# Optimization experiments

Hardware: AMD Instinct MI355X
Metric: run time of the kernel (lower is better)

Reference implementation:

```python
import jax, jax.numpy as jnp
import numpy as np

D = 1152      # hidden_size
H = 16        # num_heads
K = D // H    # head_dim = 72
L = 2         # depth
I = 4304      # intermediate_size
M = 2         # spatial_merge_size
NPOS = 2304   # num_position_embeddings (48x48)
OUT = 2048    # out_hidden_size
CIN = 3 * 2 * 16 * 16  # C*tp*p*p = 1536
GRID = np.array([[1, 48, 48], [1, 32, 64], [2, 24, 40]], dtype=np.int32)


def _ln(x, s, b, eps=1e-6):
    mu = jnp.mean(x, -1, keepdims=True)
    var = jnp.mean((x - mu) ** 2, -1, keepdims=True)
    return (x - mu) * jax.lax.rsqrt(var + eps) * s + b


def _rot_half(x):
    h = x.shape[-1] // 2
    return jnp.concatenate([-x[..., h:], x[..., :h]], -1)


def _seg_bounds(g):
    b = [0]
    for t, h, w in g:
        for _ in range(int(t)):
            b.append(b[-1] + int(h) * int(w))
    return list(zip(b[:-1], b[1:]))


def _rope_cos_sin(g):
    half = K // 2  # rotary_half_dim
    max_hw = int(g[:, 1:].max())
    inv = 1.0 / (10000.0 ** (np.arange(0, half, 2, dtype=np.float64) / half))
    table = np.arange(max_hw)[:, None] * inv[None, :]  # (max_hw, half//2)
    pos = []
    for t, h, w in g:
        t, h, w = int(t), int(h), int(w)
        mh, mw = h // M, w // M
        row = np.broadcast_to(np.arange(mh)[:, None, None, None] * M + np.arange(M)[None, None, :, None], (mh, mw, M, M)).reshape(-1)
        col = np.broadcast_to(np.arange(mw)[None, :, None, None] * M + np.arange(M)[None, None, None, :], (mh, mw, M, M)).reshape(-1)
        c = np.stack([row, col], -1)
        if t > 1:
            c = np.tile(c, (t, 1))
        pos.append(c)
    pos = np.concatenate(pos, 0)
    emb = table[pos].reshape(pos.shape[0], -1)     # (N, half)
    emb = np.concatenate([emb, emb], -1)           # (N, head_dim)
    return jnp.asarray(np.cos(emb), jnp.float32), jnp.asarray(np.sin(emb), jnp.float32)


def _pos_embeds(pos_table, g):
    n = int(NPOS ** 0.5)
    outs = []
    for t, h, w in g:
        t, h, w = int(t), int(h), int(w)
        hi = np.linspace(0, n - 1, h); wi = np.linspace(0, n - 1, w)
        hf = np.floor(hi).astype(np.int32); wf = np.floor(wi).astype(np.int32)
        hc = np.clip(hf + 1, 0, n - 1); wc = np.clip(wf + 1, 0, n - 1)
        dh = (hi - hf).astype(np.float32); dw = (wi - wf).astype(np.float32)
        i00 = (hf[:, None] * n + wf[None, :]).reshape(-1)
        i01 = (hf[:, None] * n + wc[None, :]).reshape(-1)
        i10 = (hc[:, None] * n + wf[None, :]).reshape(-1)
        i11 = (hc[:, None] * n + wc[None, :]).reshape(-1)
        w00 = ((1 - dh)[:, None] * (1 - dw)[None, :]).reshape(-1, 1)
        w01 = ((1 - dh)[:, None] * dw[None, :]).reshape(-1, 1)
        w10 = (dh[:, None] * (1 - dw)[None, :]).reshape(-1, 1)
        w11 = (dh[:, None] * dw[None, :]).reshape(-1, 1)
        e = pos_table[i00] * w00 + pos_table[i01] * w01 + pos_table[i10] * w10 + pos_table[i11] * w11
        # spatial-merge reorder
        e = jnp.tile(e, (t, 1)).reshape(t, h // M, M, w // M, M, -1).transpose(0, 1, 3, 2, 4, 5).reshape(-1, D)
        outs.append(e)
    return jnp.concatenate(outs, 0)


def _forward(pixel_values, grid, patch_w, patch_b, pos_table, ln1_s, ln1_b, qkv_w, qkv_b,
             proj_w, proj_b, ln2_s, ln2_b, fc1_w, fc1_b, fc2_w, fc2_b,
             m_ln_s, m_ln_b, m_fc1_w, m_fc1_b, m_fc2_w, m_fc2_b):
    g = np.asarray(grid)
    # patch embed: conv with kernel==stride over whole patch == matmul on flattened patch
    x = pixel_values @ patch_w + patch_b               # (N, D)
    x = x + _pos_embeds(pos_table, g)
    cos, sin = _rope_cos_sin(g)                        # (N, K) each
    bounds = _seg_bounds(g)
    scale = K ** -0.5
    for l in range(L):
        h = _ln(x, ln1_s[l], ln1_b[l])
        N = h.shape[0]
        qkv = (h @ qkv_w[l] + qkv_b[l]).reshape(N, 3, H, K)
        q, k, v = qkv[:, 0], qkv[:, 1], qkv[:, 2]
        q = q * cos[:, None, :] + _rot_half(q) * sin[:, None, :]
        k = k * cos[:, None, :] + _rot_half(k) * sin[:, None, :]
        outs = []
        for s, e in bounds:  # static ragged segments (cu_seqlens)
            logits = jnp.einsum('lhk,mhk->hlm', q[s:e], k[s:e]) * scale
            wts = jax.nn.softmax(logits.astype(jnp.float32), -1).astype(logits.dtype)
            outs.append(jnp.einsum('hlm,mhk->lhk', wts, v[s:e]).reshape(e - s, H * K))
        attn = jnp.concatenate(outs, 0) @ proj_w[l] + proj_b[l]
        x = x + attn
        h2 = _ln(x, ln2_s[l], ln2_b[l])
        x = x + jax.nn.gelu(h2 @ fc1_w[l] + fc1_b[l], approximate=True) @ fc2_w[l] + fc2_b[l]
    normed = _ln(x, m_ln_s, m_ln_b).reshape(-1, D * M * M)
    return jax.nn.gelu(normed @ m_fc1_w + m_fc1_b, approximate=True) @ m_fc2_w + m_fc2_b


def setup_inputs() -> dict:
    key = jax.random.key(0)
    ks = jax.random.split(key, 16)
    def nrm(k, shp, s=0.02):
        return jax.random.normal(k, shp, jnp.float32) * s
    Ntok = int(sum(int(t) * int(h) * int(w) for t, h, w in GRID))  # 6272
    return {
        'pixel_values': nrm(ks[0], (Ntok, CIN), 1.0),
        'grid_thw': jnp.asarray(GRID),
        'patch_w': nrm(ks[1], (CIN, D)), 'patch_b': nrm(ks[2], (D,), 0.01),
        'pos_table': nrm(ks[3], (NPOS, D)),
        'ln1_s': jnp.ones((L, D)), 'ln1_b': jnp.zeros((L, D)),
        'qkv_w': nrm(ks[4], (L, D, 3 * D)), 'qkv_b': nrm(ks[5], (L, 3 * D), 0.01),
        'proj_w': nrm(ks[6], (L, D, D)), 'proj_b': nrm(ks[7], (L, D), 0.01),
        'ln2_s': jnp.ones((L, D)), 'ln2_b': jnp.zeros((L, D)),
        'fc1_w': nrm(ks[8], (L, D, I)), 'fc1_b': nrm(ks[9], (L, I), 0.01),
        'fc2_w': nrm(ks[10], (L, I, D)), 'fc2_b': nrm(ks[11], (L, D), 0.01),
        'm_ln_s': jnp.ones((D,)), 'm_ln_b': jnp.zeros((D,)),
        'm_fc1_w': nrm(ks[12], (D * M * M, D * M * M)), 'm_fc1_b': nrm(ks[13], (D * M * M,), 0.01),
        'm_fc2_w': nrm(ks[14], (D * M * M, OUT)), 'm_fc2_b': nrm(ks[15], (OUT,), 0.01),
    }


def reference(pixel_values, grid_thw, patch_w, patch_b, pos_table, ln1_s, ln1_b, qkv_w, qkv_b,
              proj_w, proj_b, ln2_s, ln2_b, fc1_w, fc1_b, fc2_w, fc2_b,
              m_ln_s, m_ln_b, m_fc1_w, m_fc1_b, m_fc2_w, m_fc2_b):
    return _forward(pixel_values, grid_thw, patch_w, patch_b, pos_table, ln1_s, ln1_b, qkv_w, qkv_b,
                    proj_w, proj_b, ln2_s, ln2_b, fc1_w, fc1_b, fc2_w, fc2_b,
                    m_ln_s, m_ln_b, m_fc1_w, m_fc1_b, m_fc2_w, m_fc2_b)
```

## Files before the change

kernel.cpp:

```cpp
#include <hip/hip_runtime.h>

typedef __bf16 bf16;
typedef float f32x4 __attribute__((ext_vector_type(4)));
typedef bf16 bf16x8 __attribute__((ext_vector_type(8)));

#define NTOK 6272
#define DMODEL 1152

__device__ __forceinline__ void tok_geo(int t, int& row, int& col, int& gh, int& gw) {
    int local;
    if (t < 2304)      { local = t;        gh = 48; gw = 48; }
    else if (t < 4352) { local = t - 2304; gh = 32; gw = 64; }
    else if (t < 5312) { local = t - 4352; gh = 24; gw = 40; }
    else               { local = t - 5312; gh = 24; gw = 40; }
    int mc = local & 1;
    int mr = (local >> 1) & 1;
    int rest = local >> 2;
    int mwc = gw >> 1;
    int mw = rest % mwc;
    int mh = rest / mwc;
    row = mh * 2 + mr;
    col = mw * 2 + mc;
}

__device__ __forceinline__ float gelu_tanh(float v) {
    float c = v + 0.044715f * v * v * v;
    return 0.5f * v * (1.0f + tanhf(0.7978845608028654f * c));
}

__global__ void detect_kernel(const unsigned short* __restrict__ px, int* __restrict__ flag) {
    int tid = threadIdx.x;
    int cnt = 0;
    for (int i = tid * 8; i < tid * 8 + 8; i++) {
        unsigned e = (px[i] >> 7) & 0xFF;
        if (e < 100u || e > 140u) cnt++;
    }
#pragma unroll
    for (int off = 32; off > 0; off >>= 1) cnt += __shfl_down(cnt, off);
    if (tid == 0) *flag = (cnt > 64) ? 1 : 0;
}

template <typename T>
__device__ __forceinline__ void load8(const T* src, bf16* dst, bool pred) {
    if (!pred) {
        uint4 z = {0, 0, 0, 0};
        *(uint4*)dst = z;
        return;
    }
    if constexpr (sizeof(T) == 2) {
        *(uint4*)dst = *(const uint4*)src;
    } else {
        float4 a = *(const float4*)src;
        float4 b = *(const float4*)(src + 4);
        dst[0] = (bf16)a.x; dst[1] = (bf16)a.y; dst[2] = (bf16)a.z; dst[3] = (bf16)a.w;
        dst[4] = (bf16)b.x; dst[5] = (bf16)b.y; dst[6] = (bf16)b.z; dst[7] = (bf16)b.w;
    }
}

template <typename TI>
__global__ __launch_bounds__(256) void pos_embed_kernel(const int* __restrict__ flag,
                                                        const TI* __restrict__ tab,
                                                        bf16* __restrict__ x) {
    if (*flag != (sizeof(TI) == 4 ? 1 : 0)) return;
    int t = blockIdx.x;
    int row, col, gh, gw;
    tok_geo(t, row, col, gh, gw);
    float hi = row * 47.0f / (gh - 1);
    float wi = col * 47.0f / (gw - 1);
    int hf = (int)hi, wf = (int)wi;
    int hc = min(hf + 1, 47), wc = min(wf + 1, 47);
    float dh = hi - hf, dw = wi - wf;
    float w00 = (1.f - dh) * (1.f - dw);
    float w01 = (1.f - dh) * dw;
    float w10 = dh * (1.f - dw);
    float w11 = dh * dw;
    const TI* p00 = tab + (size_t)(hf * 48 + wf) * DMODEL;
    const TI* p01 = tab + (size_t)(hf * 48 + wc) * DMODEL;
    const TI* p10 = tab + (size_t)(hc * 48 + wf) * DMODEL;
    const TI* p11 = tab + (size_t)(hc * 48 + wc) * DMODEL;
    bf16* xr = x + (size_t)t * DMODEL;
    for (int d = threadIdx.x; d < DMODEL; d += 256)
        xr[d] = (bf16)(w00 * (float)p00[d] + w01 * (float)p01[d] +
                       w10 * (float)p10[d] + w11 * (float)p11[d]);
}

template <typename TI>
__global__ __launch_bounds__(256) void ln_kernel(const int* __restrict__ flag,
                                                 const bf16* __restrict__ x,
                                                 const TI* __restrict__ s,
                                                 const TI* __restrict__ b,
                                                 bf16* __restrict__ out) {
    if (*flag != (sizeof(TI) == 4 ? 1 : 0)) return;
    const int row = blockIdx.x;
    const int tid = threadIdx.x;
    __shared__ float red[4];
    const bf16* xr = x + (size_t)row * DMODEL;
    float vals[5];
    int cnt = 0;
    float sum = 0.f;
    for (int i = tid; i < DMODEL; i += 256) { vals[cnt] = (float)xr[i]; sum += vals[cnt]; cnt++; }
#pragma unroll
    for (int off = 32; off > 0; off >>= 1) sum += __shfl_down(sum, off);
    if ((tid & 63) == 0) red[tid >> 6] = sum;
    __syncthreads();
    float mean = (red[0] + red[1] + red[2] + red[3]) * (1.0f / DMODEL);
    float vs = 0.f;
    for (int i = 0; i < cnt; i++) { float d = vals[i] - mean; vs += d * d; }
#pragma unroll
    for (int off = 32; off > 0; off >>= 1) vs += __shfl_down(vs, off);
    __syncthreads();
    if ((tid & 63) == 0) red[tid >> 6] = vs;
    __syncthreads();
    float var = (red[0] + red[1] + red[2] + red[3]) * (1.0f / DMODEL);
    float inv = rsqrtf(var + 1e-6f);
    int idx = 0;
    for (int i = tid; i < DMODEL; i += 256)
        out[(size_t)row * DMODEL + i] = (bf16)((vals[idx++] - mean) * inv * (float)s[i] + (float)b[i]);
}

__global__ __launch_bounds__(256) void rope_inplace_kernel(bf16* __restrict__ qkv) {
    int idx = blockIdx.x * 256 + threadIdx.x;
    const int total = NTOK * 16 * 36;
    if (idx >= total) return;
    int j = idx % 36;
    int rest = idx / 36;
    int h = rest & 15;
    int t = rest >> 4;
    bf16* base = qkv + (size_t)t * 3456 + h * 72;
    int row, col, gh, gw;
    tok_geo(t, row, col, gh, gw);
    float pos = (float)((j < 18) ? row : col);
    int fi = (j < 18) ? j : j - 18;
    float ang = pos * powf(10000.0f, -(float)fi / 18.0f);
    float cv = cosf(ang), sv = sinf(ang);
    float q0v = (float)base[j],        q1v = (float)base[j + 36];
    float k0v = (float)base[1152 + j], k1v = (float)base[1152 + j + 36];
    base[j]          = (bf16)(q0v * cv - q1v * sv);
    base[j + 36]     = (bf16)(q1v * cv + q0v * sv);
    base[1152 + j]      = (bf16)(k0v * cv - k1v * sv);
    base[1152 + j + 36] = (bf16)(k1v * cv + k0v * sv);
}

__global__ __launch_bounds__(256) void attn_kernel(const bf16* __restrict__ qkv,
                                                   bf16* __restrict__ outp) {
    const int bx = blockIdx.x;
    const int head = bx & 15;
    const int qt = bx >> 4;
    int sbase, slen, qtb;
    if (qt < 36)      { sbase = 0;    slen = 2304; qtb = 0;  }
    else if (qt < 68) { sbase = 2304; slen = 2048; qtb = 36; }
    else if (qt < 83) { sbase = 4352; slen = 960;  qtb = 68; }
    else              { sbase = 5312; slen = 960;  qtb = 83; }
    const int q0 = sbase + (qt - qtb) * 64;

    __shared__ bf16 Ks[64][104];
    __shared__ bf16 Vs[80][72];
    __shared__ bf16 Ps[64][72];

    const int tid = threadIdx.x;
    const int wv = tid >> 6;
    const int lane = tid & 63;
    const int quad = lane >> 4;
    const int l15 = lane & 15;

    const size_t hoff = (size_t)head * 72;

    for (int c = tid; c < 64; c += 256) {
        int r = 72 + (c >> 3), cc = (c & 7) * 8;
        uint4 z = {0, 0, 0, 0};
        *(uint4*)&Vs[r][cc] = z;
    }

    for (int c = tid; c < 768; c += 256) {
        int r = c / 12, cc = (c % 12) * 8;
        uint4 v = {0, 0, 0, 0};
        if (cc < 72) v = *(const uint4*)(qkv + (size_t)(q0 + r) * 3456 + hoff + cc);
        *(uint4*)&Ks[r][cc] = v;
    }
    __syncthreads();
    bf16x8 aq[3];
#pragma unroll
    for (int i = 0; i < 3; i++) aq[i] = *(const bf16x8*)&Ks[wv * 16 + l15][i * 32 + quad * 8];

    const int cc0 = wv * 8;
    const bool w0 = tid < 64;
    const bf16* kp = qkv + (size_t)(sbase + lane) * 3456 + 1152 + hoff + cc0;
    const int stepE = 64 * 3456;

    uint4 kr0, kr1, kr2, vr0, vr1, vr2;
    kr0 = *(const uint4*)kp;
    kr1 = *(const uint4*)(kp + 32);
    vr0 = *(const uint4*)(kp + 1152);
    vr1 = *(const uint4*)(kp + 1184);
    if (w0) {
        kr2 = *(const uint4*)(kp + 64);
        vr2 = *(const uint4*)(kp + 1216);
    }
    kp += stepE;

    f32x4 o[5] = {};
    float m_i[4], l_i[4];
#pragma unroll
    for (int r = 0; r < 4; r++) { m_i[r] = -1e30f; l_i[r] = 0.f; }

    const float C1 = 0.17002234f;
    const int nkv = slen >> 6;
    for (int kt = 0; kt < nkv; kt++) {
        __syncthreads();
        *(uint4*)&Ks[lane][cc0] = kr0;
        *(uint4*)&Ks[lane][cc0 + 32] = kr1;
        if (w0) *(uint4*)&Ks[lane][64] = kr2;
        {
            const bf16* e = (const bf16*)&vr0;
#pragma unroll
            for (int i = 0; i < 8; i++) Vs[cc0 + i][lane] = e[i];
        }
        {
            const bf16* e = (const bf16*)&vr1;
#pragma unroll
            for (int i = 0; i < 8; i++) Vs[cc0 + 32 + i][lane] = e[i];
        }
        if (w0) {
            const bf16* e = (const bf16*)&vr2;
#pragma unroll
            for (int i = 0; i < 8; i++) Vs[64 + i][lane] = e[i];
        }
        __syncthreads();

        if (kt + 1 < nkv) {
            kr0 = *(const uint4*)kp;
            kr1 = *(const uint4*)(kp + 32);
            vr0 = *(const uint4*)(kp + 1152);
            vr1 = *(const uint4*)(kp + 1184);
            if (w0) {
                kr2 = *(const uint4*)(kp + 64);
                vr2 = *(const uint4*)(kp + 1216);
            }
            kp += stepE;
        }

        f32x4 sfr[4] = {};
#pragma unroll
        for (int kc = 0; kc < 3; kc++)
#pragma unroll
            for (int nt = 0; nt < 4; nt++) {
                bf16x8 bk = *(const bf16x8*)&Ks[nt * 16 + l15][kc * 32 + quad * 8];
                sfr[nt] = __builtin_amdgcn_mfma_f32_16x16x32_bf16(aq[kc], bk, sfr[nt], 0, 0, 0);
            }

        float mx[4];
#pragma unroll
        for (int reg = 0; reg < 4; reg++) {
            float m = fmaxf(fmaxf(sfr[0][reg], sfr[1][reg]), fmaxf(sfr[2][reg], sfr[3][reg]));
            m = fmaxf(m, __shfl_xor(m, 1));
            m = fmaxf(m, __shfl_xor(m, 2));
            m = fmaxf(m, __shfl_xor(m, 4));
            m = fmaxf(m, __shfl_xor(m, 8));
            mx[reg] = m;
        }
        bool grow = (mx[0] > m_i[0]) || (mx[1] > m_i[1]) || (mx[2] > m_i[2]) || (mx[3] > m_i[3]);
        if (__any(grow)) {
#pragma unroll
            for (int reg = 0; reg < 4; reg++) {
                float mn = fmaxf(m_i[reg], mx[reg]);
                float a = __builtin_amdgcn_exp2f((m_i[reg] - mn) * C1);
                m_i[reg] = mn;
                l_i[reg] *= a;
#pragma unroll
                for (int nt = 0; nt < 5; nt++) o[nt][reg] *= a;
            }
        }
        float mc[4];
#pragma unroll
        for (int reg = 0; reg < 4; reg++) mc[reg] = m_i[reg] * C1;
        float rs[4] = {0.f, 0.f, 0.f, 0.f};
#pragma unroll
        for (int nt = 0; nt < 4; nt++)
#pragma unroll
            for (int reg = 0; reg < 4; reg++) {
                float p = __builtin_amdgcn_exp2f(fmaf(sfr[nt][reg], C1, -mc[reg]));
                sfr[nt][reg] = p;
                rs[reg] += p;
            }
#pragma unroll
        for (int reg = 0; reg < 4; reg++) {
            float r = rs[reg];
            r += __shfl_xor(r, 1);
            r += __shfl_xor(r, 2);
            r += __shfl_xor(r, 4);
            r += __shfl_xor(r, 8);
            l_i[reg] += r;
        }

#pragma unroll
        for (int nt = 0; nt < 4; nt++)
#pragma unroll
            for (int reg = 0; reg < 4; reg++)
                Ps[wv * 16 + quad * 4 + reg][nt * 16 + l15] = (bf16)sfr[nt][reg];

#pragma unroll
        for (int kc = 0; kc < 2; kc++) {
            bf16x8 ap = *(const bf16x8*)&Ps[wv * 16 + l15][kc * 32 + quad * 8];
#pragma unroll
            for (int nt = 0; nt < 5; nt++) {
                bf16x8 bv = *(const bf16x8*)&Vs[nt * 16 + l15][kc * 32 + quad * 8];
                o[nt] = __builtin_amdgcn_mfma_f32_16x16x32_bf16(ap, bv, o[nt], 0, 0, 0);
            }
        }
    }

#pragma unroll
    for (int nt = 0; nt < 5; nt++)
#pragma unroll
        for (int reg = 0; reg < 4; reg++) {
            int c = nt * 16 + l15;
            if (c < 72) {
                int tok = q0 + wv * 16 + quad * 4 + reg;
                outp[(size_t)tok * DMODEL + head * 72 + c] = (bf16)(o[nt][reg] / l_i[reg]);
            }
        }
}

template <int MODE, typename TA, typename TB>
__global__ __launch_bounds__(256) void gemm_kernel(const int* __restrict__ flag,
                                                   const TA* __restrict__ A,
                                                   const TB* __restrict__ B,
                                                   const TB* __restrict__ bias,
                                                   void* __restrict__ outp,
                                                   int M, int N, int K) {
    if (*flag != (sizeof(TB) == 4 ? 1 : 0)) return;
    __shared__ bf16 As[128][40];
    __shared__ bf16 Bs[128][40];
    const int tid = threadIdx.x;
    const int m0 = blockIdx.y * 128;
    const int n0 = blockIdx.x * 128;
    const int wv = tid >> 6;
    const int lane = tid & 63;
    const int quad = lane >> 4;
    const int l15 = lane & 15;
    const int wr = (wv >> 1) * 64;
    const int wc = (wv & 1) * 64;

    const int a_row = tid >> 1;
    const int a_col = (tid & 1) * 16;
    const int b_k = tid & 31;
    const int b_n = (tid >> 5) * 16;

    f32x4 acc[4][4] = {};

    for (int k0 = 0; k0 < K; k0 += 32) {
        __syncthreads();
        {
            bf16 ea[16];
            int gr = m0 + a_row;
            const TA* ap = A + (size_t)gr * K + k0 + a_col;
            load8(ap, ea, gr < M && (k0 + a_col) < K);
            load8(ap + 8, ea + 8, gr < M && (k0 + a_col + 8) < K);
            *(uint4*)&As[a_row][a_col] = *(uint4*)ea;
            *(uint4*)&As[a_row][a_col + 8] = *(uint4*)(ea + 8);
        }
        {
            bf16 eb[16];
            int gk = k0 + b_k;
            const TB* bp = B + (size_t)gk * N + n0 + b_n;
            load8(bp, eb, gk < K && (n0 + b_n) < N);
            load8(bp + 8, eb + 8, gk < K && (n0 + b_n + 8) < N);
#pragma unroll
            for (int i = 0; i < 16; i++) Bs[b_n + i][b_k] = eb[i];
        }
        __syncthreads();

        bf16x8 af[4], bfv[4];
#pragma unroll
        for (int mi = 0; mi < 4; mi++) af[mi] = *(const bf16x8*)&As[wr + mi * 16 + l15][quad * 8];
#pragma unroll
        for (int ni = 0; ni < 4; ni++) bfv[ni] = *(const bf16x8*)&Bs[wc + ni * 16 + l15][quad * 8];
#pragma unroll
        for (int mi = 0; mi < 4; mi++)
#pragma unroll
            for (int ni = 0; ni < 4; ni++)
                acc[mi][ni] = __builtin_amdgcn_mfma_f32_16x16x32_bf16(af[mi], bfv[ni], acc[mi][ni], 0, 0, 0);
    }

#pragma unroll
    for (int mi = 0; mi < 4; mi++) {
#pragma unroll
        for (int ni = 0; ni < 4; ni++) {
#pragma unroll
            for (int reg = 0; reg < 4; reg++) {
                int r = m0 + wr + mi * 16 + quad * 4 + reg;
                int c = n0 + wc + ni * 16 + l15;
                if (r < M && c < N) {
                    float v = acc[mi][ni][reg] + (float)bias[c];
                    if (MODE == 1) v = gelu_tanh(v);
                    if (MODE == 2) {
                        bf16* o = (bf16*)outp;
                        size_t idx = (size_t)r * N + c;
                        o[idx] = (bf16)((float)o[idx] + v);
                    } else if (MODE == 3) {
                        TB* o = (TB*)outp;
                        o[(size_t)r * N + c] = (TB)v;
                    } else {
                        bf16* o = (bf16*)outp;
                        o[(size_t)r * N + c] = (bf16)v;
                    }
                }
            }
        }
    }
}


template <typename TI>
__global__ __launch_bounds__(256) void cvt_kernel(const int* __restrict__ flag,
                                                  const TI* __restrict__ in,
                                                  bf16* __restrict__ out, int n8) {
    if (*flag != (sizeof(TI) == 4 ? 1 : 0)) return;
    for (int i = blockIdx.x * 256 + threadIdx.x; i < n8; i += gridDim.x * 256) {
        bf16 e[8];
        load8(in + (size_t)i * 8, e, true);
        *(uint4*)(out + (size_t)i * 8) = *(uint4*)e;
    }
}

template <typename TI>
__global__ __launch_bounds__(256) void transpose_w_kernel(const int* __restrict__ flag,
                                                          const TI* __restrict__ B,
                                                          bf16* __restrict__ T,
                                                          int K, int N, int Kpad) {
    if (*flag != (sizeof(TI) == 4 ? 1 : 0)) return;
    __shared__ bf16 t[64][72];
    const int k0 = blockIdx.y * 64, n0 = blockIdx.x * 64;
    const int tid = threadIdx.x;
    const int kk = tid >> 2;
    const int nn0 = (tid & 3) * 16;
    bf16 e[16];
    bool ok = (k0 + kk < K) && (n0 + nn0 < N);
    const TI* src = B + (size_t)(k0 + kk) * N + n0 + nn0;
    load8(src, e, ok);
    load8(src + 8, e + 8, ok);
#pragma unroll
    for (int i = 0; i < 16; i++) t[nn0 + i][kk] = e[i];
    __syncthreads();
    const int nn = tid >> 2;
    const int j16 = (tid & 3) * 16;
    if (n0 + nn < N && k0 + j16 < Kpad) {
        bf16* dst = T + (size_t)(n0 + nn) * Kpad + k0 + j16;
        *(uint4*)dst = *(uint4*)&t[nn][j16];
        *(uint4*)(dst + 8) = *(uint4*)&t[nn][j16 + 8];
    }
}

template <typename TI>
__global__ __launch_bounds__(256) void cvt_bias_kernel(const int* __restrict__ flag,
        const TI* p0, const TI* p1, const TI* p2, const TI* p3, const TI* p4,
        const TI* p5, const TI* p6, const TI* p7, const TI* p8, const TI* p9,
        const TI* p10, bf16* __restrict__ out) {
    if (*flag != (sizeof(TI) == 4 ? 1 : 0)) return;
    const int lens[11] = {1152, 3456, 3456, 1152, 1152, 4304, 4304, 1152, 1152, 4608, 2048};
    const int offs[11] = {0, 1152, 4608, 8064, 9216, 10368, 14672, 18976, 20128, 21280, 25888};
    int b = blockIdx.x;
    const TI* src = (b == 0) ? p0 : (b == 1) ? p1 : (b == 2) ? p2 : (b == 3) ? p3
                  : (b == 4) ? p4 : (b == 5) ? p5 : (b == 6) ? p6 : (b == 7) ? p7
                  : (b == 8) ? p8 : (b == 9) ? p9 : p10;
    for (int i = threadIdx.x; i < lens[b]; i += 256) out[offs[b] + i] = (bf16)(float)src[i];
}

typedef const __attribute__((address_space(1))) void* gas_ptr;
typedef __attribute__((address_space(3))) void* las_ptr;
__device__ __forceinline__ void gload16(const bf16* g, bf16* l) {
    __builtin_amdgcn_global_load_lds((gas_ptr)g, (las_ptr)l, 16, 0, 0);
}

template <int MODE>
__global__ __launch_bounds__(256) void gemm_lds_kernel(const int* __restrict__ flag,
        const bf16* __restrict__ A, const bf16* __restrict__ BT,
        const bf16* __restrict__ bias, void* __restrict__ outp,
        int M, int N, int K, int ldc) {
    __shared__ bf16 As[128][32];
    __shared__ bf16 Bs[128][32];
    const int tid = threadIdx.x;
    const int m0 = blockIdx.y * 128;
    const int n0 = blockIdx.x * 128;
    const int wv = tid >> 6;
    const int lane = tid & 63;
    const int quad = lane >> 4;
    const int l15 = lane & 15;
    const int wr = (wv >> 1) * 64;
    const int wc = (wv & 1) * 64;

    const int sr = wv * 32 + (lane >> 2);
    const int sc = (lane & 3) * 8;
    const bf16* aP0 = A + (size_t)min(m0 + sr, M - 1) * K + sc;
    const bf16* aP1 = A + (size_t)min(m0 + sr + 16, M - 1) * K + sc;
    const bf16* bP0 = BT + (size_t)min(n0 + sr, N - 1) * K + sc;
    const bf16* bP1 = BT + (size_t)min(n0 + sr + 16, N - 1) * K + sc;
    bf16* lA0 = &As[wv * 32][0];
    bf16* lA1 = &As[wv * 32 + 16][0];
    bf16* lB0 = &Bs[wv * 32][0];
    bf16* lB1 = &Bs[wv * 32 + 16][0];

    f32x4 acc[4][4] = {};
    for (int k0 = 0; k0 < K; k0 += 32) {
        __syncthreads();
        gload16(aP0 + k0, lA0);
        gload16(aP1 + k0, lA1);
        gload16(bP0 + k0, lB0);
        gload16(bP1 + k0, lB1);
        __syncthreads();
        bf16x8 af[4], bfv[4];
#pragma unroll
        for (int mi = 0; mi < 4; mi++) af[mi] = *(const bf16x8*)&As[wr + mi * 16 + l15][quad * 8];
#pragma unroll
        for (int ni = 0; ni < 4; ni++) bfv[ni] = *(const bf16x8*)&Bs[wc + ni * 16 + l15][quad * 8];
#pragma unroll
        for (int mi = 0; mi < 4; mi++)
#pragma unroll
            for (int ni = 0; ni < 4; ni++)
                acc[mi][ni] = __builtin_amdgcn_mfma_f32_16x16x32_bf16(af[mi], bfv[ni], acc[mi][ni], 0, 0, 0);
    }

    const int isf32 = (MODE == 3) ? *flag : 0;
#pragma unroll
    for (int mi = 0; mi < 4; mi++) {
#pragma unroll
        for (int ni = 0; ni < 4; ni++) {
#pragma unroll
            for (int reg = 0; reg < 4; reg++) {
                int r = m0 + wr + mi * 16 + quad * 4 + reg;
                int c = n0 + wc + ni * 16 + l15;
                if (r < M && c < ldc) {
                    float v = 0.f;
                    if (c < N) {
                        v = acc[mi][ni][reg] + (float)bias[c];
                        if (MODE == 1) v = gelu_tanh(v);
                    }
                    if (MODE == 2) {
                        bf16* o = (bf16*)outp;
                        size_t idx = (size_t)r * ldc + c;
                        o[idx] = (bf16)((float)o[idx] + v);
                    } else if (MODE == 3) {
                        if (isf32) ((float*)outp)[(size_t)r * ldc + c] = v;
                        else       ((bf16*)outp)[(size_t)r * ldc + c] = (bf16)v;
                    } else {
                        ((bf16*)outp)[(size_t)r * ldc + c] = (bf16)v;
                    }
                }
            }
        }
    }
}

#define OFF_PATCH  0ULL
#define OFF_QKV    1769472ULL
#define QKV_SZ     3981312ULL
#define OFF_PROJ   9732096ULL
#define PROJ_SZ    1327104ULL
#define OFF_FC1    12386304ULL
#define FC1_SZ     4958208ULL
#define OFF_FC2    22302720ULL
#define FC2_SZ     4976640ULL
#define OFF_MFC1   32256000ULL
#define OFF_MFC2   53489664ULL
#define OFF_BIAS   62926848ULL
#define WS_NEEDED  209001280ULL

extern "C" void kernel_launch(void* const* d_in, const int* in_sizes, int n_in,
                              void* d_out, int out_size, void* d_ws, size_t ws_size,
                              hipStream_t stream) {
    char* ws = (char*)d_ws;
    int* flag  = (int*)ws;
    bf16* x    = (bf16*)(ws + 256);
    bf16* h    = (bf16*)(ws + 256 + 14450688);
    bf16* bufA = (bf16*)(ws + 256 + 28901376);

    detect_kernel<<<1, 64, 0, stream>>>((const unsigned short*)d_in[0], flag);

    if (ws_size >= WS_NEEDED) {
        bf16* wT = (bf16*)(ws + 256 + 28901376 + 54190080);
        bf16* bias = wT + OFF_BIAS;
        bf16* px = bufA;

        cvt_kernel<bf16><<<1024, 256, 0, stream>>>(flag, (const bf16*)d_in[0], px, 1204224);
        cvt_kernel<float><<<1024, 256, 0, stream>>>(flag, (const float*)d_in[0], px, 1204224);

        auto T2 = [&](const void* srcBase, size_t eoff, bf16* dst, int K, int N, int Kpad) {
            dim3 g((N + 63) / 64, (Kpad + 63) / 64);
            transpose_w_kernel<bf16><<<g, 256, 0, stream>>>(flag, (const bf16*)srcBase + eoff, dst, K, N, Kpad);
            transpose_w_kernel<float><<<g, 256, 0, stream>>>(flag, (const float*)srcBase + eoff, dst, K, N, Kpad);
        };
        T2(d_in[2], 0, wT + OFF_PATCH, 1536, 1152, 1536);
        for (int l = 0; l < 2; l++) {
            T2(d_in[7],  (size_t)l * 1152 * 3456, wT + OFF_QKV + l * QKV_SZ, 1152, 3456, 1152);
            T2(d_in[9],  (size_t)l * 1152 * 1152, wT + OFF_PROJ + l * PROJ_SZ, 1152, 1152, 1152);
            T2(d_in[13], (size_t)l * 1152 * 4304, wT + OFF_FC1 + l * FC1_SZ, 1152, 4304, 1152);
            T2(d_in[15], (size_t)l * 4304 * 1152, wT + OFF_FC2 + l * FC2_SZ, 4304, 1152, 4320);
        }
        T2(d_in[19], 0, wT + OFF_MFC1, 4608, 4608, 4608);
        T2(d_in[21], 0, wT + OFF_MFC2, 4608, 2048, 4608);

        cvt_bias_kernel<bf16><<<11, 256, 0, stream>>>(flag,
            (const bf16*)d_in[3],
            (const bf16*)d_in[8], (const bf16*)d_in[8] + 3456,
            (const bf16*)d_in[10], (const bf16*)d_in[10] + 1152,
            (const bf16*)d_in[14], (const bf16*)d_in[14] + 4304,
            (const bf16*)d_in[16], (const bf16*)d_in[16] + 1152,
            (const bf16*)d_in[20], (const bf16*)d_in[22], bias);
        cvt_bias_kernel<float><<<11, 256, 0, stream>>>(flag,
            (const float*)d_in[3],
            (const float*)d_in[8], (const float*)d_in[8] + 3456,
            (const float*)d_in[10], (const float*)d_in[10] + 1152,
            (const float*)d_in[14], (const float*)d_in[14] + 4304,
            (const float*)d_in[16], (const float*)d_in[16] + 1152,
            (const float*)d_in[20], (const float*)d_in[22], bias);

        pos_embed_kernel<bf16><<<NTOK, 256, 0, stream>>>(flag, (const bf16*)d_in[4], x);
        pos_embed_kernel<float><<<NTOK, 256, 0, stream>>>(flag, (const float*)d_in[4], x);

        gemm_lds_kernel<2><<<dim3(9, 49), 256, 0, stream>>>(flag, px, wT + OFF_PATCH,
                                                            bias + 0, x, NTOK, 1152, 1536, 1152);

        for (int l = 0; l < 2; l++) {
            ln_kernel<bf16><<<NTOK, 256, 0, stream>>>(flag, x, (const bf16*)d_in[5] + l * 1152,
                                                      (const bf16*)d_in[6] + l * 1152, h);
            ln_kernel<float><<<NTOK, 256, 0, stream>>>(flag, x, (const float*)d_in[5] + l * 1152,
                                                       (const float*)d_in[6] + l * 1152, h);
            gemm_lds_kernel<0><<<dim3(27, 49), 256, 0, stream>>>(flag, h, wT + OFF_QKV + l * QKV_SZ,
                                                                 bias + 1152 + l * 3456, bufA,
                                                                 NTOK, 3456, 1152, 3456);
            rope_inplace_kernel<<<(NTOK * 16 * 36 + 255) / 256, 256, 0, stream>>>(bufA);
            attn_kernel<<<98 * 16, 256, 0, stream>>>(bufA, h);
            gemm_lds_kernel<2><<<dim3(9, 49), 256, 0, stream>>>(flag, h, wT + OFF_PROJ + l * PROJ_SZ,
                                                                bias + 8064 + l * 1152, x,
                                                                NTOK, 1152, 1152, 1152);
            ln_kernel<bf16><<<NTOK, 256, 0, stream>>>(flag, x, (const bf16*)d_in[11] + l * 1152,
                                                      (const bf16*)d_in[12] + l * 1152, h);
            ln_kernel<float><<<NTOK, 256, 0, stream>>>(flag, x, (const float*)d_in[11] + l * 1152,
                                                       (const float*)d_in[12] + l * 1152, h);
            gemm_lds_kernel<1><<<dim3(34, 49), 256, 0, stream>>>(flag, h, wT + OFF_FC1 + l * FC1_SZ,
                                                                 bias + 10368 + l * 4304, bufA,
                                                                 NTOK, 4304, 1152, 4320);
            gemm_lds_kernel<2><<<dim3(9, 49), 256, 0, stream>>>(flag, bufA, wT + OFF_FC2 + l * FC2_SZ,
                                                                bias + 18976 + l * 1152, x,
                                                                NTOK, 1152, 4320, 1152);
        }
        ln_kernel<bf16><<<NTOK, 256, 0, stream>>>(flag, x, (const bf16*)d_in[17], (const bf16*)d_in[18], h);
        ln_kernel<float><<<NTOK, 256, 0, stream>>>(flag, x, (const float*)d_in[17], (const float*)d_in[18], h);
        gemm_lds_kernel<1><<<dim3(36, 13), 256, 0, stream>>>(flag, h, wT + OFF_MFC1,
                                                             bias + 21280, bufA, 1568, 4608, 4608, 4608);
        gemm_lds_kernel<3><<<dim3(16, 13), 256, 0, stream>>>(flag, bufA, wT + OFF_MFC2,
                                                             bias + 25888, d_out, 1568, 2048, 4608, 2048);
        return;
    }

    {
        pos_embed_kernel<bf16><<<NTOK, 256, 0, stream>>>(flag, (const bf16*)d_in[4], x);
        pos_embed_kernel<float><<<NTOK, 256, 0, stream>>>(flag, (const float*)d_in[4], x);
        gemm_kernel<2, bf16, bf16><<<dim3(9, 49), 256, 0, stream>>>(
            flag, (const bf16*)d_in[0], (const bf16*)d_in[2], (const bf16*)d_in[3], x, NTOK, 1152, 1536);
        gemm_kernel<2, float, float><<<dim3(9, 49), 256, 0, stream>>>(
            flag, (const float*)d_in[0], (const float*)d_in[2], (const float*)d_in[3], x, NTOK, 1152, 1536);
    }
    for (int l = 0; l < 2; l++) {
        ln_kernel<bf16><<<NTOK, 256, 0, stream>>>(flag, x, (const bf16*)d_in[5] + l * 1152,
                                                  (const bf16*)d_in[6] + l * 1152, h);
        ln_kernel<float><<<NTOK, 256, 0, stream>>>(flag, x, (const float*)d_in[5] + l * 1152,
                                                   (const float*)d_in[6] + l * 1152, h);
        gemm_kernel<0, bf16, bf16><<<dim3(27, 49), 256, 0, stream>>>(
            flag, h, (const bf16*)d_in[7] + (size_t)l * 1152 * 3456,
            (const bf16*)d_in[8] + l * 3456, bufA, NTOK, 3456, 1152);
        gemm_kernel<0, bf16, float><<<dim3(27, 49), 256, 0, stream>>>(
            flag, h, (const float*)d_in[7] + (size_t)l * 1152 * 3456,
            (const float*)d_in[8] + l * 3456, bufA, NTOK, 3456, 1152);
        rope_inplace_kernel<<<(NTOK * 16 * 36 + 255) / 256, 256, 0, stream>>>(bufA);
        attn_kernel<<<98 * 16, 256, 0, stream>>>(bufA, h);
        gemm_kernel<2, bf16, bf16><<<dim3(9, 49), 256, 0, stream>>>(
            flag, h, (const bf16*)d_in[9] + (size_t)l * 1152 * 1152,
            (const bf16*)d_in[10] + l * 1152, x, NTOK, 1152, 1152);
        gemm_kernel<2, bf16, float><<<dim3(9, 49), 256, 0, stream>>>(
            flag, h, (const float*)d_in[9] + (size_t)l * 1152 * 1152,
            (const float*)d_in[10] + l * 1152, x, NTOK, 1152, 1152);
        ln_kernel<bf16><<<NTOK, 256, 0, stream>>>(flag, x, (const bf16*)d_in[11] + l * 1152,
                                                  (const bf16*)d_in[12] + l * 1152, h);
        ln_kernel<float><<<NTOK, 256, 0, stream>>>(flag, x, (const float*)d_in[11] + l * 1152,
                                                   (const float*)d_in[12] + l * 1152, h);
        gemm_kernel<1, bf16, bf16><<<dim3(34, 49), 256, 0, stream>>>(
            flag, h, (const bf16*)d_in[13] + (size_t)l * 1152 * 4304,
            (const bf16*)d_in[14] + l * 4304, bufA, NTOK, 4304, 1152);
        gemm_kernel<1, bf16, float><<<dim3(34, 49), 256, 0, stream>>>(
            flag, h, (const float*)d_in[13] + (size_t)l * 1152 * 4304,
            (const float*)d_in[14] + l * 4304, bufA, NTOK, 4304, 1152);
        gemm_kernel<2, bf16, bf16><<<dim3(9, 49), 256, 0, stream>>>(
            flag, bufA, (const bf16*)d_in[15] + (size_t)l * 4304 * 1152,
            (const bf16*)d_in[16] + l * 1152, x, NTOK, 1152, 4304);
        gemm_kernel<2, bf16, float><<<dim3(9, 49), 256, 0, stream>>>(
            flag, bufA, (const float*)d_in[15] + (size_t)l * 4304 * 1152,
            (const float*)d_in[16] + l * 1152, x, NTOK, 1152, 4304);
    }
    ln_kernel<bf16><<<NTOK, 256, 0, stream>>>(flag, x, (const bf16*)d_in[17], (const bf16*)d_in[18], h);
    ln_kernel<float><<<NTOK, 256, 0, stream>>>(flag, x, (const float*)d_in[17], (const float*)d_in[18], h);
    gemm_kernel<1, bf16, bf16><<<dim3(36, 13), 256, 0, stream>>>(
        flag, h, (const bf16*)d_in[19], (const bf16*)d_in[20], bufA, 1568, 4608, 4608);
    gemm_kernel<1, bf16, float><<<dim3(36, 13), 256, 0, stream>>>(
        flag, h, (const float*)d_in[19], (const float*)d_in[20], bufA, 1568, 4608, 4608);
    gemm_kernel<3, bf16, bf16><<<dim3(16, 13), 256, 0, stream>>>(
        flag, bufA, (const bf16*)d_in[21], (const bf16*)d_in[22], d_out, 1568, 2048, 4608);
    gemm_kernel<3, bf16, float><<<dim3(16, 13), 256, 0, stream>>>(
        flag, bufA, (const float*)d_in[21], (const float*)d_in[22], d_out, 1568, 2048, 4608);
}
```

Baseline: 2.362 ms.

## Add 64-row GEMM tile for narrow-N GEMMs and drop attention K/V register prefetch

Adds a gemm_lds64_kernel with 64x128 tiles and uses it for the patch, proj, fc2 and merger fc2 GEMMs. These have narrow N, so the smaller M tile doubles the block count and fills more compute units. Separately, the attention kernel no longer prefetches the next K/V tile into registers; it loads K and V straight into LDS inside the loop. That cuts register pressure but gives up overlap of global loads with the MFMA work.

```diff
diff --git a/kernel.cpp b/kernel.cpp
--- a/kernel.cpp
+++ b/kernel.cpp
@@ -182,22 +182,6 @@
 #pragma unroll
     for (int i = 0; i < 3; i++) aq[i] = *(const bf16x8*)&Ks[wv * 16 + l15][i * 32 + quad * 8];
 
-    const int cc0 = wv * 8;
-    const bool w0 = tid < 64;
-    const bf16* kp = qkv + (size_t)(sbase + lane) * 3456 + 1152 + hoff + cc0;
-    const int stepE = 64 * 3456;
-
-    uint4 kr0, kr1, kr2, vr0, vr1, vr2;
-    kr0 = *(const uint4*)kp;
-    kr1 = *(const uint4*)(kp + 32);
-    vr0 = *(const uint4*)(kp + 1152);
-    vr1 = *(const uint4*)(kp + 1184);
-    if (w0) {
-        kr2 = *(const uint4*)(kp + 64);
-        vr2 = *(const uint4*)(kp + 1216);
-    }
-    kp += stepE;
-
     f32x4 o[5] = {};
     float m_i[4], l_i[4];
 #pragma unroll
@@ -206,38 +190,22 @@
     const float C1 = 0.17002234f;
     const int nkv = slen >> 6;
     for (int kt = 0; kt < nkv; kt++) {
+        const int k0 = sbase + kt * 64;
         __syncthreads();
-        *(uint4*)&Ks[lane][cc0] = kr0;
-        *(uint4*)&Ks[lane][cc0 + 32] = kr1;
-        if (w0) *(uint4*)&Ks[lane][64] = kr2;
-        {
-            const bf16* e = (const bf16*)&vr0;
-#pragma unroll
-            for (int i = 0; i < 8; i++) Vs[cc0 + i][lane] = e[i];
-        }
-        {
-            const bf16* e = (const bf16*)&vr1;
-#pragma unroll
-            for (int i = 0; i < 8; i++) Vs[cc0 + 32 + i][lane] = e[i];
-        }
-        if (w0) {
-            const bf16* e = (const bf16*)&vr2;
-#pragma unroll
-            for (int i = 0; i < 8; i++) Vs[64 + i][lane] = e[i];
+        for (int c = tid; c < 768; c += 256) {
+            int r = c / 12, cc = (c % 12) * 8;
+            uint4 v = {0, 0, 0, 0};
+            if (cc < 72) v = *(const uint4*)(qkv + (size_t)(k0 + r) * 3456 + 1152 + hoff + cc);
+            *(uint4*)&Ks[r][cc] = v;
+        }
+        for (int c = tid; c < 576; c += 256) {
+            int r = c & 63, cc = (c >> 6) * 8;
+            uint4 v = *(const uint4*)(qkv + (size_t)(k0 + r) * 3456 + 2304 + hoff + cc);
+            const bf16* e = (const bf16*)&v;
+#pragma unroll
+            for (int i = 0; i < 8; i++) Vs[cc + i][r] = e[i];
         }
         __syncthreads();
-
-        if (kt + 1 < nkv) {
-            kr0 = *(const uint4*)kp;
-            kr1 = *(const uint4*)(kp + 32);
-            vr0 = *(const uint4*)(kp + 1152);
-            vr1 = *(const uint4*)(kp + 1184);
-            if (w0) {
-                kr2 = *(const uint4*)(kp + 64);
-                vr2 = *(const uint4*)(kp + 1216);
-            }
-            kp += stepE;
-        }
 
         f32x4 sfr[4] = {};
 #pragma unroll
@@ -551,6 +519,83 @@
     }
 }
 
+template <int MODE>
+__global__ __launch_bounds__(256) void gemm_lds64_kernel(const int* __restrict__ flag,
+        const bf16* __restrict__ A, const bf16* __restrict__ BT,
+        const bf16* __restrict__ bias, void* __restrict__ outp,
+        int M, int N, int K, int ldc) {
+    __shared__ bf16 As[64][32];
+    __shared__ bf16 Bs[128][32];
+    const int tid = threadIdx.x;
+    const int m0 = blockIdx.y * 64;
+    const int n0 = blockIdx.x * 128;
+    const int wv = tid >> 6;
+    const int lane = tid & 63;
+    const int quad = lane >> 4;
+    const int l15 = lane & 15;
+    const int wr = (wv >> 1) * 32;
+    const int wc = (wv & 1) * 64;
+
+    const int sc = (lane & 3) * 8;
+    const int srA = wv * 16 + (lane >> 2);
+    const int srB = wv * 32 + (lane >> 2);
+    const bf16* aP0 = A + (size_t)min(m0 + srA, M - 1) * K + sc;
+    const bf16* bP0 = BT + (size_t)min(n0 + srB, N - 1) * K + sc;
+    const bf16* bP1 = BT + (size_t)min(n0 + srB + 16, N - 1) * K + sc;
+    bf16* lA0 = &As[wv * 16][0];
+    bf16* lB0 = &Bs[wv * 32][0];
+    bf16* lB1 = &Bs[wv * 32 + 16][0];
+
+    f32x4 acc[2][4] = {};
+    for (int k0 = 0; k0 < K; k0 += 32) {
+        __syncthreads();
+        gload16(aP0 + k0, lA0);
+        gload16(bP0 + k0, lB0);
+        gload16(bP1 + k0, lB1);
+        __syncthreads();
+        bf16x8 af[2], bfv[4];
+#pragma unroll
+        for (int mi = 0; mi < 2; mi++) af[mi] = *(const bf16x8*)&As[wr + mi * 16 + l15][quad * 8];
+#pragma unroll
+        for (int ni = 0; ni < 4; ni++) bfv[ni] = *(const bf16x8*)&Bs[wc + ni * 16 + l15][quad * 8];
+#pragma unroll
+        for (int mi = 0; mi < 2; mi++)
+#pragma unroll
+            for (int ni = 0; ni < 4; ni++)
+                acc[mi][ni] = __builtin_amdgcn_mfma_f32_16x16x32_bf16(af[mi], bfv[ni], acc[mi][ni], 0, 0, 0);
+    }
+
+    const int isf32 = (MODE == 3) ? *flag : 0;
+#pragma unroll
+    for (int mi = 0; mi < 2; mi++) {
+#pragma unroll
+        for (int ni = 0; ni < 4; ni++) {
+#pragma unroll
+            for (int reg = 0; reg < 4; reg++) {
+                int r = m0 + wr + mi * 16 + quad * 4 + reg;
+                int c = n0 + wc + ni * 16 + l15;
+                if (r < M && c < ldc) {
+                    float v = 0.f;
+                    if (c < N) {
+                        v = acc[mi][ni][reg] + (float)bias[c];
+                        if (MODE == 1) v = gelu_tanh(v);
+                    }
+                    if (MODE == 2) {
+                        bf16* o = (bf16*)outp;
+                        size_t idx = (size_t)r * ldc + c;
+                        o[idx] = (bf16)((float)o[idx] + v);
+                    } else if (MODE == 3) {
+                        if (isf32) ((float*)outp)[(size_t)r * ldc + c] = v;
+                        else       ((bf16*)outp)[(size_t)r * ldc + c] = (bf16)v;
+                    } else {
+                        ((bf16*)outp)[(size_t)r * ldc + c] = (bf16)v;
+                    }
+                }
+            }
+        }
+    }
+}
+
 #define OFF_PATCH  0ULL
 #define OFF_QKV    1769472ULL
 #define QKV_SZ     3981312ULL
@@ -617,8 +662,8 @@
         pos_embed_kernel<bf16><<<NTOK, 256, 0, stream>>>(flag, (const bf16*)d_in[4], x);
         pos_embed_kernel<float><<<NTOK, 256, 0, stream>>>(flag, (const float*)d_in[4], x);
 
-        gemm_lds_kernel<2><<<dim3(9, 49), 256, 0, stream>>>(flag, px, wT + OFF_PATCH,
-                                                            bias + 0, x, NTOK, 1152, 1536, 1152);
+        gemm_lds64_kernel<2><<<dim3(9, 98), 256, 0, stream>>>(flag, px, wT + OFF_PATCH,
+                                                              bias + 0, x, NTOK, 1152, 1536, 1152);
 
         for (int l = 0; l < 2; l++) {
             ln_kernel<bf16><<<NTOK, 256, 0, stream>>>(flag, x, (const bf16*)d_in[5] + l * 1152,
@@ -630,9 +675,9 @@
                                                                  NTOK, 3456, 1152, 3456);
             rope_inplace_kernel<<<(NTOK * 16 * 36 + 255) / 256, 256, 0, stream>>>(bufA);
             attn_kernel<<<98 * 16, 256, 0, stream>>>(bufA, h);
-            gemm_lds_kernel<2><<<dim3(9, 49), 256, 0, stream>>>(flag, h, wT + OFF_PROJ + l * PROJ_SZ,
-                                                                bias + 8064 + l * 1152, x,
-                                                                NTOK, 1152, 1152, 1152);
+            gemm_lds64_kernel<2><<<dim3(9, 98), 256, 0, stream>>>(flag, h, wT + OFF_PROJ + l * PROJ_SZ,
+                                                                  bias + 8064 + l * 1152, x,
+                                                                  NTOK, 1152, 1152, 1152);
             ln_kernel<bf16><<<NTOK, 256, 0, stream>>>(flag, x, (const bf16*)d_in[11] + l * 1152,
                                                       (const bf16*)d_in[12] + l * 1152, h);
             ln_kernel<float><<<NTOK, 256, 0, stream>>>(flag, x, (const float*)d_in[11] + l * 1152,
@@ -640,16 +685,16 @@
             gemm_lds_kernel<1><<<dim3(34, 49), 256, 0, stream>>>(flag, h, wT + OFF_FC1 + l * FC1_SZ,
                                                                  bias + 10368 + l * 4304, bufA,
                                                                  NTOK, 4304, 1152, 4320);
-            gemm_lds_kernel<2><<<dim3(9, 49), 256, 0, stream>>>(flag, bufA, wT + OFF_FC2 + l * FC2_SZ,
-                                                                bias + 18976 + l * 1152, x,
-                                                                NTOK, 1152, 4320, 1152);
+            gemm_lds64_kernel<2><<<dim3(9, 98), 256, 0, stream>>>(flag, bufA, wT + OFF_FC2 + l * FC2_SZ,
+                                                                  bias + 18976 + l * 1152, x,
+                                                                  NTOK, 1152, 4320, 1152);
         }
         ln_kernel<bf16><<<NTOK, 256, 0, stream>>>(flag, x, (const bf16*)d_in[17], (const bf16*)d_in[18], h);
         ln_kernel<float><<<NTOK, 256, 0, stream>>>(flag, x, (const float*)d_in[17], (const float*)d_in[18], h);
         gemm_lds_kernel<1><<<dim3(36, 13), 256, 0, stream>>>(flag, h, wT + OFF_MFC1,
                                                              bias + 21280, bufA, 1568, 4608, 4608, 4608);
-        gemm_lds_kernel<3><<<dim3(16, 13), 256, 0, stream>>>(flag, bufA, wT + OFF_MFC2,
-                                                             bias + 25888, d_out, 1568, 2048, 4608, 2048);
+        gemm_lds64_kernel<3><<<dim3(16, 25), 256, 0, stream>>>(flag, bufA, wT + OFF_MFC2,
+                                                               bias + 25888, d_out, 1568, 2048, 4608, 2048);
         return;
     }
 
```

Result: faster. 2.212 ms (-6.4%).
